# Optimization experiments

Measured on AMD Instinct MI355X. Metric: run time of the kernel, lower is better.

Reference implementation:

```python
import jax, jax.numpy as jnp
import numpy as np

IN_FEATURES = 4096
OUT_FEATURES = 4096
N_TOKENS = 8192


def setup_inputs() -> dict:
    key = jax.random.key(0)
    kx, kw = jax.random.split(key)
    x = jax.random.normal(kx, (N_TOKENS, IN_FEATURES), dtype=jnp.float32)
    # weight = randn(out, in) * 0.1, bias = zeros(out), per BinaryLinear.__init__
    weight = jax.random.normal(kw, (OUT_FEATURES, IN_FEATURES), dtype=jnp.float32) * 0.1
    bias = jnp.zeros((OUT_FEATURES,), dtype=jnp.float32)
    return {"x": x, "weight": weight, "bias": bias}


def reference(x, weight, bias):
    # sign-binarize weights (torch .sign(): -1/0/+1, matched by jnp.sign),
    # then dense linear: x @ sign(W)^T + b
    bin_w = jnp.sign(weight)
    return jnp.einsum('ni,oi->no', x, bin_w) + bias
```

## Files before the change

kernel.cpp:

```cpp
#include <hip/hip_runtime.h>
#include <stdint.h>

typedef __attribute__((ext_vector_type(4)))  int i32x4;
typedef __attribute__((ext_vector_type(16))) int i32x16;

#define M_TOK 8192
#define N_OUT 4096
#define K_IN  4096

#define BM 256
#define BN 256
#define BKB 64
#define NT (K_IN / BKB)
#define SLOT_BYTES 32768
#define B_OFF 16384

#define GLDS16(gp, lp)                                                         \
  __builtin_amdgcn_global_load_lds(                                            \
      (const __attribute__((address_space(1))) void*)(gp),                     \
      (__attribute__((address_space(3))) void*)(lp), 16, 0, 0)

__global__ void __launch_bounds__(256) quant_x_i8(const float* __restrict__ x,
                                                  char* __restrict__ xq,
                                                  float* __restrict__ scales) {
  const int row = blockIdx.x;
  const int t   = threadIdx.x;
  const float4* rp = (const float4*)(x + (size_t)row * K_IN);

  float4 v[4];
#pragma unroll
  for (int p = 0; p < 4; p++) v[p] = rp[p * 256 + t];

  float amax = 0.f;
#pragma unroll
  for (int p = 0; p < 4; p++)
    amax = fmaxf(amax, fmaxf(fmaxf(fabsf(v[p].x), fabsf(v[p].y)),
                             fmaxf(fabsf(v[p].z), fabsf(v[p].w))));

#pragma unroll
  for (int off = 32; off > 0; off >>= 1)
    amax = fmaxf(amax, __shfl_xor(amax, off));

  __shared__ float wmax[4];
  if ((t & 63) == 0) wmax[t >> 6] = amax;
  __syncthreads();
  amax = fmaxf(fmaxf(wmax[0], wmax[1]), fmaxf(wmax[2], wmax[3]));
  amax = fmaxf(amax, 1e-30f);

  const float inv = 127.f / amax;
  if (t == 0) scales[row] = amax / 127.f;

  uint32_t* op = (uint32_t*)(xq + (size_t)row * K_IN);
#pragma unroll
  for (int p = 0; p < 4; p++) {
    uint32_t b0 = (uint32_t)(__float2int_rn(v[p].x * inv) & 0xFF);
    uint32_t b1 = (uint32_t)(__float2int_rn(v[p].y * inv) & 0xFF);
    uint32_t b2 = (uint32_t)(__float2int_rn(v[p].z * inv) & 0xFF);
    uint32_t b3 = (uint32_t)(__float2int_rn(v[p].w * inv) & 0xFF);
    op[p * 256 + t] = b0 | (b1 << 8) | (b2 << 16) | (b3 << 24);
  }
}

__global__ void __launch_bounds__(256) quant_w_sign(const float* __restrict__ w,
                                                    char* __restrict__ wq) {
  const int t = threadIdx.x;
  const size_t base = (size_t)blockIdx.x * 1024;
  const float4* p = (const float4*)w + base;
  uint32_t* op = (uint32_t*)wq + base;
#pragma unroll
  for (int q = 0; q < 4; q++) {
    float4 f = p[q * 256 + t];
    int s0 = (f.x > 0.f) - (f.x < 0.f);
    int s1 = (f.y > 0.f) - (f.y < 0.f);
    int s2 = (f.z > 0.f) - (f.z < 0.f);
    int s3 = (f.w > 0.f) - (f.w < 0.f);
    op[q * 256 + t] = (uint32_t)(s0 & 0xFF) | ((uint32_t)(s1 & 0xFF) << 8) |
                      ((uint32_t)(s2 & 0xFF) << 16) | ((uint32_t)(s3 & 0xFF) << 24);
  }
}

__global__ void __launch_bounds__(512, 2) gemm_bin_i8(
    const char* __restrict__ A, const char* __restrict__ B,
    const float* __restrict__ scales, const float* __restrict__ bias,
    float* __restrict__ C) {
  __shared__ __align__(16) char lds[4 * SLOT_BYTES];

  const int tid  = threadIdx.x;
  const int lane = tid & 63;
  const int wv   = tid >> 6;
  const int wm   = wv >> 2;
  const int wn   = wv & 3;

  int bid = (int)blockIdx.x;
  bid = (bid & 7) * (512 >> 3) + (bid >> 3);
  const int m0 = (bid >> 4) * BM;
  const int n0 = (bid & 15) * BN;

  const int srow   = lane >> 2;
  const int schunk = (lane & 3) ^ ((lane >> 3) & 3);
  const char* gAb = A + (size_t)(m0 + wv * 32 + srow) * K_IN + schunk * 16;
  const char* gBb = B + (size_t)(n0 + wv * 32 + srow) * K_IN + schunk * 16;
  char* lAb = lds + wv * 2048;
  char* lBb = lds + B_OFF + wv * 2048;

  auto stage = [&](int tt, int sl) {
    const size_t ko = (size_t)tt * BKB;
    GLDS16(gAb + ko,                     lAb + sl * SLOT_BYTES);
    GLDS16(gAb + ko + (size_t)16 * K_IN, lAb + sl * SLOT_BYTES + 1024);
    GLDS16(gBb + ko,                     lBb + sl * SLOT_BYTES);
    GLDS16(gBb + ko + (size_t)16 * K_IN, lBb + sl * SLOT_BYTES + 1024);
  };

  const int fr  = lane & 31;
  const int k16 = lane >> 5;
  const int x3  = (lane >> 1) & 3;
  const int aoff = wm * 8192 + fr * 64;
  const int boff = B_OFF + wn * 4096 + fr * 64;

  i32x16 acc[4][2];
#pragma unroll
  for (int m = 0; m < 4; m++)
#pragma unroll
    for (int n = 0; n < 2; n++)
#pragma unroll
      for (int r = 0; r < 16; r++) acc[m][n][r] = 0;

  auto compute = [&](int sl) {
    const char* pA = lds + sl * SLOT_BYTES + aoff;
    const char* pB = lds + sl * SLOT_BYTES + boff;
#pragma unroll
    for (int ks = 0; ks < 2; ks++) {
      const int so = ((2 * ks + k16) ^ x3) << 4;
      i32x4 a0 = *(const i32x4*)(pA + so);
      i32x4 a1 = *(const i32x4*)(pA + 2048 + so);
      i32x4 a2 = *(const i32x4*)(pA + 4096 + so);
      i32x4 a3 = *(const i32x4*)(pA + 6144 + so);
      i32x4 b0 = *(const i32x4*)(pB + so);
      i32x4 b1 = *(const i32x4*)(pB + 2048 + so);
      __builtin_amdgcn_s_setprio(1);
      acc[0][0] = __builtin_amdgcn_mfma_i32_32x32x32_i8(a0, b0, acc[0][0], 0, 0, 0);
      acc[0][1] = __builtin_amdgcn_mfma_i32_32x32x32_i8(a0, b1, acc[0][1], 0, 0, 0);
      acc[1][0] = __builtin_amdgcn_mfma_i32_32x32x32_i8(a1, b0, acc[1][0], 0, 0, 0);
      acc[1][1] = __builtin_amdgcn_mfma_i32_32x32x32_i8(a1, b1, acc[1][1], 0, 0, 0);
      acc[2][0] = __builtin_amdgcn_mfma_i32_32x32x32_i8(a2, b0, acc[2][0], 0, 0, 0);
      acc[2][1] = __builtin_amdgcn_mfma_i32_32x32x32_i8(a2, b1, acc[2][1], 0, 0, 0);
      acc[3][0] = __builtin_amdgcn_mfma_i32_32x32x32_i8(a3, b0, acc[3][0], 0, 0, 0);
      acc[3][1] = __builtin_amdgcn_mfma_i32_32x32x32_i8(a3, b1, acc[3][1], 0, 0, 0);
      __builtin_amdgcn_s_setprio(0);
    }
  };

  stage(0, 0);
  stage(1, 1);
  stage(2, 2);

  for (int t = 0; t < NT - 3; ++t) {
    asm volatile("s_waitcnt vmcnt(8)" ::: "memory");
    __builtin_amdgcn_s_barrier();
    __builtin_amdgcn_sched_barrier(0);
    stage(t + 3, (t + 3) & 3);
    compute(t & 3);
  }
  asm volatile("s_waitcnt vmcnt(8)" ::: "memory");
  __builtin_amdgcn_s_barrier();
  __builtin_amdgcn_sched_barrier(0);
  compute((NT - 3) & 3);
  asm volatile("s_waitcnt vmcnt(4)" ::: "memory");
  __builtin_amdgcn_s_barrier();
  __builtin_amdgcn_sched_barrier(0);
  compute((NT - 2) & 3);
  asm volatile("s_waitcnt vmcnt(0)" ::: "memory");
  __builtin_amdgcn_s_barrier();
  __builtin_amdgcn_sched_barrier(0);
  compute((NT - 1) & 3);

  const int col0 = n0 + wn * 64 + (lane & 31);
  const float bv0 = bias[col0];
  const float bv1 = bias[col0 + 32];
#pragma unroll
  for (int m = 0; m < 4; m++) {
    const int rb = m0 + wm * 128 + m * 32 + ((lane >> 5) << 2);
#pragma unroll
    for (int r = 0; r < 16; r++) {
      const int row = rb + (r & 3) + ((r >> 2) << 3);
      const float sc = scales[row];
      float* cp = C + (size_t)row * N_OUT + col0;
      cp[0]  = (float)acc[m][0][r] * sc + bv0;
      cp[32] = (float)acc[m][1][r] * sc + bv1;
    }
  }
}

__global__ void fallback_gemm(const float* __restrict__ x, const float* __restrict__ w,
                              const float* __restrict__ bias, float* __restrict__ out) {
  int idx = blockIdx.x * blockDim.x + threadIdx.x;
  if (idx >= M_TOK * N_OUT) return;
  int row = idx / N_OUT, col = idx % N_OUT;
  const float* xp = x + (size_t)row * K_IN;
  const float* wp = w + (size_t)col * K_IN;
  float s = 0.f;
  for (int k = 0; k < K_IN; k++) {
    float wv = wp[k];
    float sg = wv > 0.f ? 1.f : (wv < 0.f ? -1.f : 0.f);
    s += xp[k] * sg;
  }
  out[idx] = s + bias[col];
}

extern "C" void kernel_launch(void* const* d_in, const int* in_sizes, int n_in,
                              void* d_out, int out_size, void* d_ws, size_t ws_size,
                              hipStream_t stream) {
  const float* x    = (const float*)d_in[0];
  const float* w    = (const float*)d_in[1];
  const float* bias = (const float*)d_in[2];
  float* out = (float*)d_out;

  const size_t xq_bytes = (size_t)M_TOK * K_IN;
  const size_t wq_bytes = (size_t)N_OUT * K_IN;
  const size_t sc_bytes = (size_t)M_TOK * sizeof(float);

  if (ws_size < xq_bytes + wq_bytes + sc_bytes) {
    int total = M_TOK * N_OUT;
    fallback_gemm<<<(total + 255) / 256, 256, 0, stream>>>(x, w, bias, out);
    return;
  }

  char*  xq = (char*)d_ws;
  char*  wq = (char*)d_ws + xq_bytes;
  float* sc = (float*)((char*)d_ws + xq_bytes + wq_bytes);

  quant_x_i8<<<M_TOK, 256, 0, stream>>>(x, xq, sc);
  quant_w_sign<<<(N_OUT * K_IN / 4) / 1024, 256, 0, stream>>>(w, wq);

  gemm_bin_i8<<<512, 512, 0, stream>>>(xq, wq, sc, bias, out);
}
```

Before: 396.1 us.

## Fuse quantization kernels and restructure GEMM into finer-grained interleaved load phases

Merges the activation-quantization and weight-sign kernels into one launch that picks its path by block index, removing a kernel launch and the gap between the two. The GEMM main loop is reorganised into half-tile phases, each issuing one A or B prefetch between LDS reads and MFMAs. Each phase has two workgroup barriers and waits on memory every two phases, with a prefetch depth of two tiles instead of three. This spreads global loads across the loop more evenly, at the cost of more barriers and a shallower prefetch.

```diff
diff --git a/kernel.cpp b/kernel.cpp
--- a/kernel.cpp
+++ b/kernel.cpp
@@ -20,62 +20,65 @@
       (const __attribute__((address_space(1))) void*)(gp),                     \
       (__attribute__((address_space(3))) void*)(lp), 16, 0, 0)
 
-__global__ void __launch_bounds__(256) quant_x_i8(const float* __restrict__ x,
-                                                  char* __restrict__ xq,
-                                                  float* __restrict__ scales) {
-  const int row = blockIdx.x;
-  const int t   = threadIdx.x;
-  const float4* rp = (const float4*)(x + (size_t)row * K_IN);
-
-  float4 v[4];
-#pragma unroll
-  for (int p = 0; p < 4; p++) v[p] = rp[p * 256 + t];
-
-  float amax = 0.f;
-#pragma unroll
-  for (int p = 0; p < 4; p++)
-    amax = fmaxf(amax, fmaxf(fmaxf(fabsf(v[p].x), fabsf(v[p].y)),
-                             fmaxf(fabsf(v[p].z), fabsf(v[p].w))));
-
-#pragma unroll
-  for (int off = 32; off > 0; off >>= 1)
-    amax = fmaxf(amax, __shfl_xor(amax, off));
-
+#define VM4 asm volatile("s_waitcnt vmcnt(4)" ::: "memory")
+#define VM0 asm volatile("s_waitcnt vmcnt(0)" ::: "memory")
+#define NOPX ((void)0)
+
+__global__ void __launch_bounds__(256) quant_fused(
+    const float* __restrict__ x, const float* __restrict__ w,
+    char* __restrict__ xq, char* __restrict__ wq, float* __restrict__ scales) {
   __shared__ float wmax[4];
-  if ((t & 63) == 0) wmax[t >> 6] = amax;
-  __syncthreads();
-  amax = fmaxf(fmaxf(wmax[0], wmax[1]), fmaxf(wmax[2], wmax[3]));
-  amax = fmaxf(amax, 1e-30f);
-
-  const float inv = 127.f / amax;
-  if (t == 0) scales[row] = amax / 127.f;
-
-  uint32_t* op = (uint32_t*)(xq + (size_t)row * K_IN);
-#pragma unroll
-  for (int p = 0; p < 4; p++) {
-    uint32_t b0 = (uint32_t)(__float2int_rn(v[p].x * inv) & 0xFF);
-    uint32_t b1 = (uint32_t)(__float2int_rn(v[p].y * inv) & 0xFF);
-    uint32_t b2 = (uint32_t)(__float2int_rn(v[p].z * inv) & 0xFF);
-    uint32_t b3 = (uint32_t)(__float2int_rn(v[p].w * inv) & 0xFF);
-    op[p * 256 + t] = b0 | (b1 << 8) | (b2 << 16) | (b3 << 24);
-  }
-}
-
-__global__ void __launch_bounds__(256) quant_w_sign(const float* __restrict__ w,
-                                                    char* __restrict__ wq) {
   const int t = threadIdx.x;
-  const size_t base = (size_t)blockIdx.x * 1024;
-  const float4* p = (const float4*)w + base;
-  uint32_t* op = (uint32_t*)wq + base;
-#pragma unroll
-  for (int q = 0; q < 4; q++) {
-    float4 f = p[q * 256 + t];
-    int s0 = (f.x > 0.f) - (f.x < 0.f);
-    int s1 = (f.y > 0.f) - (f.y < 0.f);
-    int s2 = (f.z > 0.f) - (f.z < 0.f);
-    int s3 = (f.w > 0.f) - (f.w < 0.f);
-    op[q * 256 + t] = (uint32_t)(s0 & 0xFF) | ((uint32_t)(s1 & 0xFF) << 8) |
-                      ((uint32_t)(s2 & 0xFF) << 16) | ((uint32_t)(s3 & 0xFF) << 24);
+
+  if (blockIdx.x < M_TOK) {
+    const int row = blockIdx.x;
+    const float4* rp = (const float4*)(x + (size_t)row * K_IN);
+
+    float4 v[4];
+#pragma unroll
+    for (int p = 0; p < 4; p++) v[p] = rp[p * 256 + t];
+
+    float amax = 0.f;
+#pragma unroll
+    for (int p = 0; p < 4; p++)
+      amax = fmaxf(amax, fmaxf(fmaxf(fabsf(v[p].x), fabsf(v[p].y)),
+                               fmaxf(fabsf(v[p].z), fabsf(v[p].w))));
+
+#pragma unroll
+    for (int off = 32; off > 0; off >>= 1)
+      amax = fmaxf(amax, __shfl_xor(amax, off));
+
+    if ((t & 63) == 0) wmax[t >> 6] = amax;
+    __syncthreads();
+    amax = fmaxf(fmaxf(wmax[0], wmax[1]), fmaxf(wmax[2], wmax[3]));
+    amax = fmaxf(amax, 1e-30f);
+
+    const float inv = 127.f / amax;
+    if (t == 0) scales[row] = amax / 127.f;
+
+    uint32_t* op = (uint32_t*)(xq + (size_t)row * K_IN);
+#pragma unroll
+    for (int p = 0; p < 4; p++) {
+      uint32_t b0 = (uint32_t)(__float2int_rn(v[p].x * inv) & 0xFF);
+      uint32_t b1 = (uint32_t)(__float2int_rn(v[p].y * inv) & 0xFF);
+      uint32_t b2 = (uint32_t)(__float2int_rn(v[p].z * inv) & 0xFF);
+      uint32_t b3 = (uint32_t)(__float2int_rn(v[p].w * inv) & 0xFF);
+      op[p * 256 + t] = b0 | (b1 << 8) | (b2 << 16) | (b3 << 24);
+    }
+  } else {
+    const size_t base = (size_t)(blockIdx.x - M_TOK) * 1024;
+    const float4* p = (const float4*)w + base;
+    uint32_t* op = (uint32_t*)wq + base;
+#pragma unroll
+    for (int q = 0; q < 4; q++) {
+      float4 f = p[q * 256 + t];
+      int s0 = (f.x > 0.f) - (f.x < 0.f);
+      int s1 = (f.y > 0.f) - (f.y < 0.f);
+      int s2 = (f.z > 0.f) - (f.z < 0.f);
+      int s3 = (f.w > 0.f) - (f.w < 0.f);
+      op[q * 256 + t] = (uint32_t)(s0 & 0xFF) | ((uint32_t)(s1 & 0xFF) << 8) |
+                        ((uint32_t)(s2 & 0xFF) << 16) | ((uint32_t)(s3 & 0xFF) << 24);
+    }
   }
 }
 
@@ -103,12 +106,17 @@
   char* lAb = lds + wv * 2048;
   char* lBb = lds + B_OFF + wv * 2048;
 
-  auto stage = [&](int tt, int sl) {
+  auto stageA = [&](int tt) {
     const size_t ko = (size_t)tt * BKB;
-    GLDS16(gAb + ko,                     lAb + sl * SLOT_BYTES);
-    GLDS16(gAb + ko + (size_t)16 * K_IN, lAb + sl * SLOT_BYTES + 1024);
-    GLDS16(gBb + ko,                     lBb + sl * SLOT_BYTES);
-    GLDS16(gBb + ko + (size_t)16 * K_IN, lBb + sl * SLOT_BYTES + 1024);
+    char* l = lAb + (tt & 3) * SLOT_BYTES;
+    GLDS16(gAb + ko, l);
+    GLDS16(gAb + ko + (size_t)16 * K_IN, l + 1024);
+  };
+  auto stageB = [&](int tt) {
+    const size_t ko = (size_t)tt * BKB;
+    char* l = lBb + (tt & 3) * SLOT_BYTES;
+    GLDS16(gBb + ko, l);
+    GLDS16(gBb + ko + (size_t)16 * K_IN, l + 1024);
   };
 
   const int fr  = lane & 31;
@@ -125,54 +133,54 @@
 #pragma unroll
       for (int r = 0; r < 16; r++) acc[m][n][r] = 0;
 
-  auto compute = [&](int sl) {
-    const char* pA = lds + sl * SLOT_BYTES + aoff;
-    const char* pB = lds + sl * SLOT_BYTES + boff;
-#pragma unroll
-    for (int ks = 0; ks < 2; ks++) {
-      const int so = ((2 * ks + k16) ^ x3) << 4;
-      i32x4 a0 = *(const i32x4*)(pA + so);
-      i32x4 a1 = *(const i32x4*)(pA + 2048 + so);
-      i32x4 a2 = *(const i32x4*)(pA + 4096 + so);
-      i32x4 a3 = *(const i32x4*)(pA + 6144 + so);
-      i32x4 b0 = *(const i32x4*)(pB + so);
-      i32x4 b1 = *(const i32x4*)(pB + 2048 + so);
-      __builtin_amdgcn_s_setprio(1);
-      acc[0][0] = __builtin_amdgcn_mfma_i32_32x32x32_i8(a0, b0, acc[0][0], 0, 0, 0);
-      acc[0][1] = __builtin_amdgcn_mfma_i32_32x32x32_i8(a0, b1, acc[0][1], 0, 0, 0);
-      acc[1][0] = __builtin_amdgcn_mfma_i32_32x32x32_i8(a1, b0, acc[1][0], 0, 0, 0);
-      acc[1][1] = __builtin_amdgcn_mfma_i32_32x32x32_i8(a1, b1, acc[1][1], 0, 0, 0);
-      acc[2][0] = __builtin_amdgcn_mfma_i32_32x32x32_i8(a2, b0, acc[2][0], 0, 0, 0);
-      acc[2][1] = __builtin_amdgcn_mfma_i32_32x32x32_i8(a2, b1, acc[2][1], 0, 0, 0);
-      acc[3][0] = __builtin_amdgcn_mfma_i32_32x32x32_i8(a3, b0, acc[3][0], 0, 0, 0);
-      acc[3][1] = __builtin_amdgcn_mfma_i32_32x32x32_i8(a3, b1, acc[3][1], 0, 0, 0);
-      __builtin_amdgcn_s_setprio(0);
-    }
-  };
-
-  stage(0, 0);
-  stage(1, 1);
-  stage(2, 2);
-
-  for (int t = 0; t < NT - 3; ++t) {
-    asm volatile("s_waitcnt vmcnt(8)" ::: "memory");
-    __builtin_amdgcn_s_barrier();
-    __builtin_amdgcn_sched_barrier(0);
-    stage(t + 3, (t + 3) & 3);
-    compute(t & 3);
-  }
-  asm volatile("s_waitcnt vmcnt(8)" ::: "memory");
+#define PHASE(rtile, ks, STAGE_STMT, VM_STMT)                                  \
+  {                                                                            \
+    const char* pA = lds + ((rtile) & 3) * SLOT_BYTES + aoff;                  \
+    const char* pB = lds + ((rtile) & 3) * SLOT_BYTES + boff;                  \
+    const int so = ((2 * (ks) + k16) ^ x3) << 4;                               \
+    i32x4 a0 = *(const i32x4*)(pA + so);                                       \
+    i32x4 a1 = *(const i32x4*)(pA + 2048 + so);                                \
+    i32x4 a2 = *(const i32x4*)(pA + 4096 + so);                                \
+    i32x4 a3 = *(const i32x4*)(pA + 6144 + so);                                \
+    i32x4 b0 = *(const i32x4*)(pB + so);                                       \
+    i32x4 b1 = *(const i32x4*)(pB + 2048 + so);                                \
+    STAGE_STMT;                                                                \
+    VM_STMT;                                                                   \
+    __builtin_amdgcn_sched_barrier(0);                                         \
+    __builtin_amdgcn_s_barrier();                                              \
+    __builtin_amdgcn_sched_barrier(0);                                         \
+    __builtin_amdgcn_s_setprio(1);                                             \
+    acc[0][0] = __builtin_amdgcn_mfma_i32_32x32x32_i8(a0, b0, acc[0][0], 0, 0, 0); \
+    acc[0][1] = __builtin_amdgcn_mfma_i32_32x32x32_i8(a0, b1, acc[0][1], 0, 0, 0); \
+    acc[1][0] = __builtin_amdgcn_mfma_i32_32x32x32_i8(a1, b0, acc[1][0], 0, 0, 0); \
+    acc[1][1] = __builtin_amdgcn_mfma_i32_32x32x32_i8(a1, b1, acc[1][1], 0, 0, 0); \
+    acc[2][0] = __builtin_amdgcn_mfma_i32_32x32x32_i8(a2, b0, acc[2][0], 0, 0, 0); \
+    acc[2][1] = __builtin_amdgcn_mfma_i32_32x32x32_i8(a2, b1, acc[2][1], 0, 0, 0); \
+    acc[3][0] = __builtin_amdgcn_mfma_i32_32x32x32_i8(a3, b0, acc[3][0], 0, 0, 0); \
+    acc[3][1] = __builtin_amdgcn_mfma_i32_32x32x32_i8(a3, b1, acc[3][1], 0, 0, 0); \
+    __builtin_amdgcn_s_setprio(0);                                             \
+    __builtin_amdgcn_sched_barrier(0);                                         \
+    __builtin_amdgcn_s_barrier();                                              \
+  }
+
+  stageA(0); stageB(0); stageA(1); stageB(1);
+  VM4;
+  __builtin_amdgcn_sched_barrier(0);
   __builtin_amdgcn_s_barrier();
   __builtin_amdgcn_sched_barrier(0);
-  compute((NT - 3) & 3);
-  asm volatile("s_waitcnt vmcnt(4)" ::: "memory");
-  __builtin_amdgcn_s_barrier();
-  __builtin_amdgcn_sched_barrier(0);
-  compute((NT - 2) & 3);
-  asm volatile("s_waitcnt vmcnt(0)" ::: "memory");
-  __builtin_amdgcn_s_barrier();
-  __builtin_amdgcn_sched_barrier(0);
-  compute((NT - 1) & 3);
+
+  for (int I = 0; I < 31; ++I) {
+    const int t0 = 2 * I, t1 = t0 + 1, u0 = t0 + 2, u1 = t0 + 3;
+    PHASE(t0, 0, stageA(u0), NOPX);
+    PHASE(t0, 1, stageB(u0), VM4);
+    PHASE(t1, 0, stageA(u1), NOPX);
+    PHASE(t1, 1, stageB(u1), VM4);
+  }
+  PHASE(62, 0, NOPX, NOPX);
+  PHASE(62, 1, NOPX, VM0);
+  PHASE(63, 0, NOPX, NOPX);
+  PHASE(63, 1, NOPX, NOPX);
+#undef PHASE
 
   const int col0 = n0 + wn * 64 + (lane & 31);
   const float bv0 = bias[col0];
@@ -229,8 +237,7 @@
   char*  wq = (char*)d_ws + xq_bytes;
   float* sc = (float*)((char*)d_ws + xq_bytes + wq_bytes);
 
-  quant_x_i8<<<M_TOK, 256, 0, stream>>>(x, xq, sc);
-  quant_w_sign<<<(N_OUT * K_IN / 4) / 1024, 256, 0, stream>>>(w, wq);
+  quant_fused<<<M_TOK + (N_OUT * K_IN / 4) / 1024, 256, 0, stream>>>(x, w, xq, wq, sc);
 
   gemm_bin_i8<<<512, 512, 0, stream>>>(xq, wq, sc, bias, out);
 }
```

After: 399.3 us. No clear change (+0.8%).
